# Kernel optimization log

Hardware: AMD Instinct MI355X
Metric: run time of the kernel (lower is better)

Reference implementation:

```python
import jax, jax.numpy as jnp
import numpy as np

E, S, H, D, B = 8, 64, 2048, 1024, 8192
LN_EPS = 1e-5


def setup_inputs() -> dict:
    key = jax.random.key(0)
    ks = jax.random.split(key, 12)
    n = lambda k, shape: jax.random.normal(k, shape, jnp.float32) * 0.02
    return {
        "raw_state": jax.random.normal(ks[0], (B, S), jnp.float32),
        "has_proprio": jax.random.randint(ks[1], (B,), 0, 2, jnp.int32),
        "expert_idx": jax.random.randint(ks[2], (B,), 0, E, jnp.int32),
        "pw1": n(ks[3], (E, S, H)), "pb1": jnp.zeros((E, H), jnp.float32),
        "pw2": n(ks[4], (E, H, D)), "pb2": jnp.zeros((E, D), jnp.float32),
        "qw1": n(ks[5], (E, S, H)), "qb1": jnp.zeros((E, H), jnp.float32),
        "qw2": n(ks[6], (E, H, D)), "qb2": jnp.zeros((E, D), jnp.float32),
        "ln_g": jnp.ones((E, D), jnp.float32), "ln_b": jnp.zeros((E, D), jnp.float32),
        "tw1": n(ks[7], (E, D, H)), "tb1": jnp.zeros((E, H), jnp.float32),
        "tw2": n(ks[8], (E, H, D)), "tb2": jnp.zeros((E, D), jnp.float32),
    }


def _gelu(x):
    # torch nn.GELU default = exact erf form
    return jax.nn.gelu(x, approximate=False)


def _expert_fwd(x, sel, w):
    (pw1, pb1, pw2, pb2, qw1, qb1, qw2, qb2, ln_g, ln_b, tw1, tb1, tw2, tb2) = w
    placeholder = _gelu(x @ pw1 + pb1) @ pw2 + pb2      # [B, D]
    proprio = _gelu(x @ qw1 + qb1) @ qw2 + qb2          # [B, D]
    mixed = placeholder * (1.0 - sel) + proprio * sel    # [B, D]
    mu = jnp.mean(mixed, axis=-1, keepdims=True)
    var = jnp.mean(jnp.square(mixed - mu), axis=-1, keepdims=True)
    normed = (mixed - mu) * jax.lax.rsqrt(var + LN_EPS) * ln_g + ln_b
    return _gelu(normed @ tw1 + tb1) @ tw2 + tb2         # [B, D]


def reference(raw_state, has_proprio, expert_idx,
              pw1, pb1, pw2, pb2, qw1, qb1, qw2, qb2,
              ln_g, ln_b, tw1, tb1, tw2, tb2):
    sel = has_proprio.astype(raw_state.dtype)[:, None]  # [B, 1]
    n_experts = pw1.shape[0]
    acc = jnp.zeros((raw_state.shape[0], tw2.shape[-1]), raw_state.dtype)
    # Fixed small loop over experts; rows routed via mask-select (same math
    # as the original index_select -> projector -> index_copy_).
    for e in range(n_experts):
        w = (pw1[e], pb1[e], pw2[e], pb2[e], qw1[e], qb1[e], qw2[e], qb2[e],
             ln_g[e], ln_b[e], tw1[e], tb1[e], tw2[e], tb2[e])
        oe = _expert_fwd(raw_state, sel, w)
        acc = jnp.where((expert_idx == e)[:, None], oe, acc)
    return acc[:, None, :]  # [B, 1, D]
```

## Files before the change

kernel.cpp:

```cpp
#include <hip/hip_runtime.h>
#include <math.h>

typedef unsigned short u16;
typedef unsigned int   u32;
typedef __attribute__((ext_vector_type(8))) short bh8;
typedef __attribute__((ext_vector_type(4))) float f4;

#define TM 128
#define TN 64
#define TK 32

__device__ __forceinline__ u16 f2b(float f) {
  u32 u = __builtin_bit_cast(u32, f);
  u += 0x7fffu + ((u >> 16) & 1u);
  return (u16)(u >> 16);
}
__device__ __forceinline__ float gelu_f(float x) {
  return 0.5f * x * (1.0f + erff(x * 0.70710678118654752f));
}

__device__ __forceinline__ void gl2lds16(const u16* g, u16* l) {
  __builtin_amdgcn_global_load_lds(
      (const __attribute__((address_space(1))) u32*)g,
      (__attribute__((address_space(3))) u32*)l, 16, 0, 0);
}

__global__ __launch_bounds__(128) void init_routing(int* __restrict__ R) {
  R[threadIdx.x] = 0;
}

__global__ __launch_bounds__(256) void hist_kernel(const int* __restrict__ eidx,
                                                   const int* __restrict__ hasp,
                                                   int* __restrict__ R,
                                                   int* __restrict__ grp) {
  int t = blockIdx.x * 256 + threadIdx.x;
  int g = eidx[t] * 2 + (hasp[t] != 0 ? 1 : 0);
  grp[t] = g;
  atomicAdd(&R[g], 1);
}

__global__ __launch_bounds__(64) void scan_kernel(int* __restrict__ R) {
  if (threadIdx.x == 0) {
    int* cnt = R; int* cur = R + 16; int* gs = R + 32; int* to = R + 64;
    gs[0] = 0; to[0] = 0;
    for (int g = 0; g < 16; g++) {
      gs[g + 1] = gs[g] + cnt[g];
      cur[g] = gs[g];
      to[g + 1] = to[g] + (cnt[g] + TM - 1) / TM;
    }
  }
}

__global__ __launch_bounds__(256) void scatter_kernel(const int* __restrict__ grp,
                                                      int* __restrict__ R,
                                                      int* __restrict__ perm) {
  int t = blockIdx.x * 256 + threadIdx.x;
  int g = grp[t];
  int pos = atomicAdd(&R[16 + g], 1);
  perm[pos] = t;
}

__global__ __launch_bounds__(256) void gather_kernel(const float* __restrict__ raw,
                                                     const int* __restrict__ perm,
                                                     u16* __restrict__ Xg) {
  int t = blockIdx.x * 256 + threadIdx.x;
  int pos = t >> 6, ln = t & 63;
  int orig = perm[pos];
  Xg[(size_t)pos * 64 + ln] = f2b(raw[(size_t)orig * 64 + ln]);
}

__global__ __launch_bounds__(256) void transpose_cvt(const float* __restrict__ srcP,
                                                     const float* __restrict__ srcQ,
                                                     int twoSrc, int Rr, int Cc,
                                                     u16* __restrict__ dst) {
  int m = blockIdx.z;
  const float* src = twoSrc ? (((m & 1) ? srcQ : srcP) + (size_t)(m >> 1) * Rr * Cc)
                            : (srcP + (size_t)m * Rr * Cc);
  u16* d = dst + (size_t)m * Rr * Cc;
  __shared__ u16 t[64][66];
  int c0 = blockIdx.x * 64, r0 = blockIdx.y * 64;
  int tx = threadIdx.x, ty = threadIdx.y;
#pragma unroll
  for (int i = 0; i < 16; i++) {
    int r = ty + i * 4;
    t[tx][r] = f2b(src[(size_t)(r0 + r) * Cc + c0 + tx]);
  }
  __syncthreads();
#pragma unroll
  for (int i = 0; i < 16; i++) {
    int c = ty + i * 4;
    d[(size_t)(c0 + c) * Rr + r0 + tx] = t[c][tx];
  }
}

__global__ __launch_bounds__(256)
void gemm_grouped(const u16* __restrict__ A, int lda,
                  const u16* __restrict__ W, int wShift, int K, int N,
                  const float* __restrict__ biasP, const float* __restrict__ biasQ,
                  int branchBias, int doGelu,
                  u16* __restrict__ outB, float* __restrict__ outF,
                  int doScatter, int ldo,
                  const int* __restrict__ gstart, const int* __restrict__ tileOff,
                  const int* __restrict__ perm) {
  __shared__ __align__(16) u16 As[2][TM * TK];
  __shared__ __align__(16) u16 Bs[2][TN * TK];

  int bidM = blockIdx.x;
  int tot = tileOff[16];
  if (bidM >= tot) return;
  int g = 0;
  while (g < 15 && bidM >= tileOff[g + 1]) g++;
  int rowStart = gstart[g] + (bidM - tileOff[g]) * TM;
  int rowEnd = gstart[g + 1];

  const u16* Wg = W + (size_t)(g >> wShift) * N * K;
  int e = g >> 1;
  const float* bias = ((branchBias && (g & 1)) ? biasQ : biasP) + (size_t)e * N;

  int tid = threadIdx.x;
  int lane = tid & 63;
  int wv = tid >> 6;
  int wm = (wv >> 1) * 64, wn = (wv & 1) * 32;
  int l15 = lane & 15, l4 = lane >> 4;
  int colBase = blockIdx.y * TN;

  int rsub = lane >> 2;
  int su = (lane & 3) ^ ((rsub >> 1) & 3);
  int cA = wv * 2;
  int rtA0 = cA * 16 + rsub;
  int rtA1 = rtA0 + 16;
  int rtB = wv * 16 + rsub;
  int ga0 = rowStart + rtA0; ga0 = ga0 < rowEnd ? ga0 : (rowEnd - 1);
  int ga1 = rowStart + rtA1; ga1 = ga1 < rowEnd ? ga1 : (rowEnd - 1);
  const u16* aSrc0 = A + (size_t)ga0 * lda + su * 8;
  const u16* aSrc1 = A + (size_t)ga1 * lda + su * 8;
  const u16* bSrc  = Wg + (size_t)(colBase + rtB) * K + su * 8;

  f4 acc[4][2];
#pragma unroll
  for (int i = 0; i < 4; i++)
#pragma unroll
    for (int j = 0; j < 2; j++) acc[i][j] = (f4){0.f, 0.f, 0.f, 0.f};

  int rx = (l15 >> 1) & 3;
  int ch = l4 ^ rx;
  int aBase = (wm + l15) * TK + ch * 8;
  int bBase = (wn + l15) * TK + ch * 8;

#define STAGE(buf, k0)                                                        \
  do {                                                                        \
    gl2lds16(aSrc0 + (k0), &As[(buf)][cA * 512]);                             \
    gl2lds16(aSrc1 + (k0), &As[(buf)][cA * 512 + 512]);                       \
    gl2lds16(bSrc + (k0), &Bs[(buf)][wv * 512]);                              \
  } while (0)

#define COMPUTE(buf)                                                          \
  do {                                                                        \
    bh8 a[4], b[2];                                                           \
    _Pragma("unroll")                                                         \
    for (int i = 0; i < 4; i++)                                               \
      a[i] = *reinterpret_cast<const bh8*>(&As[(buf)][aBase + i * (16 * TK)]);\
    _Pragma("unroll")                                                         \
    for (int j = 0; j < 2; j++)                                               \
      b[j] = *reinterpret_cast<const bh8*>(&Bs[(buf)][bBase + j * (16 * TK)]);\
    _Pragma("unroll")                                                         \
    for (int i = 0; i < 4; i++)                                               \
      _Pragma("unroll")                                                       \
      for (int j = 0; j < 2; j++)                                             \
        acc[i][j] = __builtin_amdgcn_mfma_f32_16x16x32_bf16(                  \
            a[i], b[j], acc[i][j], 0, 0, 0);                                  \
  } while (0)

  int nk = K / TK;
  STAGE(0, 0);
  __syncthreads();
  int cur = 0;
  for (int t = 1; t < nk; ++t) {
    STAGE(cur ^ 1, t * TK);
    COMPUTE(cur);
    __syncthreads();
    cur ^= 1;
  }
  COMPUTE(cur);

#pragma unroll
  for (int i = 0; i < 4; i++) {
#pragma unroll
    for (int r = 0; r < 4; r++) {
      int row = rowStart + wm + i * 16 + l4 * 4 + r;
      if (row < rowEnd) {
        int orow = doScatter ? perm[row] : row;
#pragma unroll
        for (int j = 0; j < 2; j++) {
          int col = colBase + wn + j * 16 + l15;
          float v = acc[i][j][r] + bias[col];
          if (doGelu) v = gelu_f(v);
          if (outF) outF[(size_t)orow * ldo + col] = v;
          else      outB[(size_t)orow * ldo + col] = f2b(v);
        }
      }
    }
  }
#undef STAGE
#undef COMPUTE
}

__global__ __launch_bounds__(256) void ln_kernel(const float* __restrict__ MIX,
                                                 u16* __restrict__ NRM,
                                                 const float* __restrict__ lng,
                                                 const float* __restrict__ lnb,
                                                 const int* __restrict__ gstart) {
  const int D = 1024;
  int pos = blockIdx.x;
  int g = 0;
  while (g < 15 && pos >= gstart[g + 1]) g++;
  int e = g >> 1;
  int tid = threadIdx.x;
  float x[4];
  float s = 0.f, s2 = 0.f;
#pragma unroll
  for (int i = 0; i < 4; i++) {
    float v = MIX[(size_t)pos * D + tid + i * 256];
    x[i] = v; s += v; s2 += v * v;
  }
#pragma unroll
  for (int off = 32; off >= 1; off >>= 1) {
    s += __shfl_down(s, off);
    s2 += __shfl_down(s2, off);
  }
  __shared__ float red[8];
  int wv = tid >> 6;
  if ((tid & 63) == 0) { red[wv] = s; red[4 + wv] = s2; }
  __syncthreads();
  if (tid == 0) {
    red[0] = red[0] + red[1] + red[2] + red[3];
    red[4] = red[4] + red[5] + red[6] + red[7];
  }
  __syncthreads();
  float mean = red[0] / D;
  float var = red[4] / D - mean * mean;
  float rstd = rsqrtf(var + 1e-5f);
#pragma unroll
  for (int i = 0; i < 4; i++) {
    int c = tid + i * 256;
    float v = (x[i] - mean) * rstd * lng[(size_t)e * D + c] + lnb[(size_t)e * D + c];
    NRM[(size_t)pos * D + c] = f2b(v);
  }
}

extern "C" void kernel_launch(void* const* d_in, const int* in_sizes, int n_in,
                              void* d_out, int out_size, void* d_ws, size_t ws_size,
                              hipStream_t stream) {
  const float* raw = (const float*)d_in[0];
  const int* hasp = (const int*)d_in[1];
  const int* eidx = (const int*)d_in[2];
  const float* pw1 = (const float*)d_in[3];  const float* pb1 = (const float*)d_in[4];
  const float* pw2 = (const float*)d_in[5];  const float* pb2 = (const float*)d_in[6];
  const float* qw1 = (const float*)d_in[7];  const float* qb1 = (const float*)d_in[8];
  const float* qw2 = (const float*)d_in[9];  const float* qb2 = (const float*)d_in[10];
  const float* lng = (const float*)d_in[11]; const float* lnb = (const float*)d_in[12];
  const float* tw1 = (const float*)d_in[13]; const float* tb1 = (const float*)d_in[14];
  const float* tw2 = (const float*)d_in[15]; const float* tb2 = (const float*)d_in[16];
  float* out = (float*)d_out;

  const int B = in_sizes[0] / 64;
  const int S = 64, H = 2048, D = 1024, E = 8;

  char* ws = (char*)d_ws;
  size_t o = 0;
  int* R    = (int*)(ws + o); o += 1024;
  int* grp  = (int*)(ws + o); o += (size_t)B * 4;
  int* perm = (int*)(ws + o); o += (size_t)B * 4;
  u16* Xg   = (u16*)(ws + o); o += (size_t)B * S * 2;
  u16* Hbuf = (u16*)(ws + o); o += (size_t)B * H * 2;
  float* MIX = (float*)(ws + o); o += (size_t)B * D * 4;
  u16* NRM  = (u16*)(ws + o); o += (size_t)B * D * 2;
  u16* W1T  = (u16*)(ws + o); o += (size_t)2 * E * S * H * 2;
  u16* WB   = (u16*)(ws + o);
  u16* T1T  = WB;
  u16* T2T  = WB + (size_t)E * D * H;

  int* gstart = R + 32;
  int* toff = R + 64;

  init_routing<<<1, 128, 0, stream>>>(R);
  hist_kernel<<<B / 256, 256, 0, stream>>>(eidx, hasp, R, grp);
  scan_kernel<<<1, 64, 0, stream>>>(R);
  scatter_kernel<<<B / 256, 256, 0, stream>>>(grp, R, perm);
  gather_kernel<<<B / 4, 256, 0, stream>>>(raw, perm, Xg);

  dim3 tb(64, 4);
  transpose_cvt<<<dim3(H / 64, S / 64, 16), tb, 0, stream>>>(pw1, qw1, 1, S, H, W1T);
  transpose_cvt<<<dim3(D / 64, H / 64, 16), tb, 0, stream>>>(pw2, qw2, 1, H, D, WB);

  const int maxT = B / TM + 16;
  gemm_grouped<<<dim3(maxT, H / TN), 256, 0, stream>>>(
      Xg, S, W1T, 0, S, H, pb1, qb1, 1, 1, Hbuf, nullptr, 0, H, gstart, toff, perm);
  gemm_grouped<<<dim3(maxT, D / TN), 256, 0, stream>>>(
      Hbuf, H, WB, 0, H, D, pb2, qb2, 1, 0, nullptr, MIX, 0, D, gstart, toff, perm);
  ln_kernel<<<B, 256, 0, stream>>>(MIX, NRM, lng, lnb, gstart);
  transpose_cvt<<<dim3(H / 64, D / 64, 8), tb, 0, stream>>>(tw1, nullptr, 0, D, H, T1T);
  transpose_cvt<<<dim3(D / 64, H / 64, 8), tb, 0, stream>>>(tw2, nullptr, 0, H, D, T2T);
  gemm_grouped<<<dim3(maxT, H / TN), 256, 0, stream>>>(
      NRM, D, T1T, 1, D, H, tb1, nullptr, 0, 1, Hbuf, nullptr, 0, H, gstart, toff, perm);
  gemm_grouped<<<dim3(maxT, D / TN), 256, 0, stream>>>(
      Hbuf, H, T2T, 1, H, D, tb2, nullptr, 0, 0, nullptr, out, 1, D, gstart, toff, perm);
}
```

Measured before the change: 631.3 us.

## Widen GEMM N tile and deepen LDS pipeline to four stages

The grouped GEMM output tile grows from 128x64 to 128x128, with each wave computing a 64x64 sub-tile, to raise MFMA work per LDS and global byte loaded. The double-buffered loop becomes a 4-deep ring of LDS buffers with three stages prefetched. Each stage is gated by explicit vmcnt waits and a single barrier. MFMA blocks run at raised wave priority via s_setprio. The cost is doubled accumulator registers and 64KB of LDS per block, which may lower occupancy, and fewer column tiles are launched.

```diff
diff --git a/kernel.cpp b/kernel.cpp
--- a/kernel.cpp
+++ b/kernel.cpp
@@ -7,8 +7,9 @@
 typedef __attribute__((ext_vector_type(4))) float f4;
 
 #define TM 128
-#define TN 64
+#define TN 128
 #define TK 32
+#define DEPTH 4
 
 __device__ __forceinline__ u16 f2b(float f) {
   u32 u = __builtin_bit_cast(u32, f);
@@ -102,8 +103,8 @@
                   int doScatter, int ldo,
                   const int* __restrict__ gstart, const int* __restrict__ tileOff,
                   const int* __restrict__ perm) {
-  __shared__ __align__(16) u16 As[2][TM * TK];
-  __shared__ __align__(16) u16 Bs[2][TN * TK];
+  __shared__ __align__(16) u16 As[DEPTH][TM * TK];
+  __shared__ __align__(16) u16 Bs[DEPTH][TN * TK];
 
   int bidM = blockIdx.x;
   int tot = tileOff[16];
@@ -120,68 +121,83 @@
   int tid = threadIdx.x;
   int lane = tid & 63;
   int wv = tid >> 6;
-  int wm = (wv >> 1) * 64, wn = (wv & 1) * 32;
+  int wm = (wv >> 1) * 64, wn = (wv & 1) * 64;
   int l15 = lane & 15, l4 = lane >> 4;
   int colBase = blockIdx.y * TN;
 
   int rsub = lane >> 2;
   int su = (lane & 3) ^ ((rsub >> 1) & 3);
   int cA = wv * 2;
-  int rtA0 = cA * 16 + rsub;
-  int rtA1 = rtA0 + 16;
-  int rtB = wv * 16 + rsub;
-  int ga0 = rowStart + rtA0; ga0 = ga0 < rowEnd ? ga0 : (rowEnd - 1);
-  int ga1 = rowStart + rtA1; ga1 = ga1 < rowEnd ? ga1 : (rowEnd - 1);
+  int rt0 = cA * 16 + rsub;
+  int rt1 = rt0 + 16;
+  int ga0 = rowStart + rt0; ga0 = ga0 < rowEnd ? ga0 : (rowEnd - 1);
+  int ga1 = rowStart + rt1; ga1 = ga1 < rowEnd ? ga1 : (rowEnd - 1);
   const u16* aSrc0 = A + (size_t)ga0 * lda + su * 8;
   const u16* aSrc1 = A + (size_t)ga1 * lda + su * 8;
-  const u16* bSrc  = Wg + (size_t)(colBase + rtB) * K + su * 8;
-
-  f4 acc[4][2];
+  const u16* bSrc0 = Wg + (size_t)(colBase + rt0) * K + su * 8;
+  const u16* bSrc1 = Wg + (size_t)(colBase + rt1) * K + su * 8;
+
+  f4 acc[4][4];
 #pragma unroll
   for (int i = 0; i < 4; i++)
 #pragma unroll
-    for (int j = 0; j < 2; j++) acc[i][j] = (f4){0.f, 0.f, 0.f, 0.f};
+    for (int j = 0; j < 4; j++) acc[i][j] = (f4){0.f, 0.f, 0.f, 0.f};
 
   int rx = (l15 >> 1) & 3;
-  int ch = l4 ^ rx;
-  int aBase = (wm + l15) * TK + ch * 8;
-  int bBase = (wn + l15) * TK + ch * 8;
+  int ch = (l4 ^ rx) * 8;
+  int aBase = (wm + l15) * TK + ch;
+  int bBase = (wn + l15) * TK + ch;
 
 #define STAGE(buf, k0)                                                        \
   do {                                                                        \
-    gl2lds16(aSrc0 + (k0), &As[(buf)][cA * 512]);                             \
-    gl2lds16(aSrc1 + (k0), &As[(buf)][cA * 512 + 512]);                       \
-    gl2lds16(bSrc + (k0), &Bs[(buf)][wv * 512]);                              \
+    u16* Ab = &As[(buf)][cA * 512];                                           \
+    u16* Bb = &Bs[(buf)][cA * 512];                                           \
+    gl2lds16(aSrc0 + (k0), Ab);                                               \
+    gl2lds16(aSrc1 + (k0), Ab + 512);                                         \
+    gl2lds16(bSrc0 + (k0), Bb);                                               \
+    gl2lds16(bSrc1 + (k0), Bb + 512);                                         \
   } while (0)
 
 #define COMPUTE(buf)                                                          \
   do {                                                                        \
-    bh8 a[4], b[2];                                                           \
+    bh8 a[4], b[4];                                                           \
     _Pragma("unroll")                                                         \
     for (int i = 0; i < 4; i++)                                               \
       a[i] = *reinterpret_cast<const bh8*>(&As[(buf)][aBase + i * (16 * TK)]);\
     _Pragma("unroll")                                                         \
-    for (int j = 0; j < 2; j++)                                               \
+    for (int j = 0; j < 4; j++)                                               \
       b[j] = *reinterpret_cast<const bh8*>(&Bs[(buf)][bBase + j * (16 * TK)]);\
+    __builtin_amdgcn_s_setprio(1);                                            \
     _Pragma("unroll")                                                         \
     for (int i = 0; i < 4; i++)                                               \
       _Pragma("unroll")                                                       \
-      for (int j = 0; j < 2; j++)                                             \
+      for (int j = 0; j < 4; j++)                                             \
         acc[i][j] = __builtin_amdgcn_mfma_f32_16x16x32_bf16(                  \
             a[i], b[j], acc[i][j], 0, 0, 0);                                  \
+    __builtin_amdgcn_s_setprio(0);                                            \
   } while (0)
 
   int nk = K / TK;
-  STAGE(0, 0);
-  __syncthreads();
-  int cur = 0;
-  for (int t = 1; t < nk; ++t) {
-    STAGE(cur ^ 1, t * TK);
-    COMPUTE(cur);
-    __syncthreads();
-    cur ^= 1;
-  }
-  COMPUTE(cur);
+  int npro = nk < 3 ? nk : 3;
+  for (int p = 0; p < npro; ++p) STAGE(p, p * TK);
+
+  int t = 0;
+  for (; t + 3 < nk; ++t) {
+    asm volatile("s_waitcnt vmcnt(8) lgkmcnt(0)" ::: "memory");
+    __builtin_amdgcn_s_barrier();
+    __builtin_amdgcn_sched_barrier(0);
+    STAGE((t + 3) & (DEPTH - 1), (t + 3) * TK);
+    COMPUTE(t & (DEPTH - 1));
+  }
+  for (; t < nk; ++t) {
+    int left = nk - 1 - t;
+    if (left >= 2)      asm volatile("s_waitcnt vmcnt(8) lgkmcnt(0)" ::: "memory");
+    else if (left == 1) asm volatile("s_waitcnt vmcnt(4) lgkmcnt(0)" ::: "memory");
+    else                asm volatile("s_waitcnt vmcnt(0) lgkmcnt(0)" ::: "memory");
+    __builtin_amdgcn_s_barrier();
+    __builtin_amdgcn_sched_barrier(0);
+    COMPUTE(t & (DEPTH - 1));
+  }
 
 #pragma unroll
   for (int i = 0; i < 4; i++) {
@@ -191,7 +207,7 @@
       if (row < rowEnd) {
         int orow = doScatter ? perm[row] : row;
 #pragma unroll
-        for (int j = 0; j < 2; j++) {
+        for (int j = 0; j < 4; j++) {
           int col = colBase + wn + j * 16 + l15;
           float v = acc[i][j][r] + bias[col];
           if (doGelu) v = gelu_f(v);
```

New measurement: 783.9 us. 1.24x slower.
